# Performance work log

Measured on AMD Instinct MI355X. Metric: run time of the kernel, lower is better.

Reference implementation:

```python
import jax, jax.numpy as jnp
import numpy as np

D_MODEL = 1024
NUM_HEAD = 16
D_K = D_MODEL // NUM_HEAD


def setup_inputs() -> dict:
    key = jax.random.key(0)
    ks = jax.random.split(key, 9)
    s = 1.0 / np.sqrt(D_MODEL)
    return {
        "x": jax.random.normal(ks[0], (2, 2048, D_MODEL), dtype=jnp.float32),
        "Wq": jax.random.normal(ks[1], (D_MODEL, D_MODEL), dtype=jnp.float32) * s,
        "bq": jax.random.normal(ks[2], (D_MODEL,), dtype=jnp.float32) * s,
        "Wk": jax.random.normal(ks[3], (D_MODEL, D_MODEL), dtype=jnp.float32) * s,
        "bk": jax.random.normal(ks[4], (D_MODEL,), dtype=jnp.float32) * s,
        "Wv": jax.random.normal(ks[5], (D_MODEL, D_MODEL), dtype=jnp.float32) * s,
        "bv": jax.random.normal(ks[6], (D_MODEL,), dtype=jnp.float32) * s,
        "Wo": jax.random.normal(ks[7], (D_MODEL, D_MODEL), dtype=jnp.float32) * s,
        "bo": jax.random.normal(ks[8], (D_MODEL,), dtype=jnp.float32) * s,
    }


def reference(x, Wq, bq, Wk, bk, Wv, bv, Wo, bo):
    B, S, _ = x.shape
    # QKV projections: [B,S,D] -> [B,H,S,d_k]
    def proj(W, b):
        y = jnp.einsum("bsd,df->bsf", x, W) + b
        return y.reshape(B, S, NUM_HEAD, D_K).transpose(0, 2, 1, 3)

    Q = proj(Wq, bq)
    K = proj(Wk, bk)
    V = proj(Wv, bv)
    scale = 1.0 / jnp.sqrt(jnp.asarray(D_K, dtype=x.dtype))
    attn = jnp.einsum("bhqd,bhkd->bhqk", Q, K) * scale  # [B,H,S,S]
    probs = jax.nn.softmax(attn, axis=-1)
    out = jnp.einsum("bhqk,bhkd->bhqd", probs, V)  # [B,H,S,d_k]
    out = out.transpose(0, 2, 1, 3).reshape(B, S, D_MODEL)
    return jnp.einsum("bsd,df->bsf", out, Wo) + bo
```

## Files before the change

### kernel.cpp

```cpp
#include <hip/hip_runtime.h>
#include <hip/hip_bf16.h>
#include <math.h>

constexpr int DM = 1024;
constexpr int NH = 16;
constexpr int DK = 64;
constexpr int SQ = 2048;
constexpr int BB = 2;
constexpr int MR = BB * SQ;

typedef short bf16x8 __attribute__((ext_vector_type(8)));
typedef float f32x4 __attribute__((ext_vector_type(4)));
typedef float f32x16 __attribute__((ext_vector_type(16)));

__device__ inline unsigned short f2bf(float f) {
  unsigned u = __float_as_uint(f);
  unsigned r = (u + 0x7fffu + ((u >> 16) & 1u)) >> 16;
  return (unsigned short)r;
}

__device__ inline int fswz(int r) { return (r & 7) ^ ((r >> 3) & 7); }
__device__ inline int swz(int r, int c) {
  return r * 64 + ((((c >> 3) ^ fswz(r)) & 7) << 3) + (c & 7);
}
__device__ inline int vswz(int d, int c) {
  int g = c >> 3;
  g = (g & 24) | ((g ^ fswz(d)) & 7);
  return d * 256 + g * 8 + (c & 7);
}

__global__ __launch_bounds__(256)
void cast_kernel(const float* __restrict__ in, unsigned short* __restrict__ out, int n8) {
  int i = blockIdx.x * 256 + threadIdx.x;
  if (i >= n8) return;
  float4 a = *(const float4*)&in[(size_t)i * 8];
  float4 b = *(const float4*)&in[(size_t)i * 8 + 4];
  ushort4 lo = {f2bf(a.x), f2bf(a.y), f2bf(a.z), f2bf(a.w)};
  ushort4 hi = {f2bf(b.x), f2bf(b.y), f2bf(b.z), f2bf(b.w)};
  *(ushort4*)&out[(size_t)i * 8] = lo;
  *(ushort4*)&out[(size_t)i * 8 + 4] = hi;
}

__global__ __launch_bounds__(256)
void transpose_cast_kernel(const float* __restrict__ W, unsigned short* __restrict__ Wt) {
  __shared__ float tl[32][33];
  const int tx = threadIdx.x & 31, ty = threadIdx.x >> 5;
  const int x0 = blockIdx.x * 32, y0 = blockIdx.y * 32;
  #pragma unroll
  for (int i = 0; i < 4; ++i)
    tl[ty + i * 8][tx] = W[(size_t)(y0 + ty + i * 8) * DM + x0 + tx];
  __syncthreads();
  #pragma unroll
  for (int i = 0; i < 4; ++i)
    Wt[(size_t)(x0 + ty + i * 8) * DM + y0 + tx] = f2bf(tl[tx][ty + i * 8]);
}

__global__ __launch_bounds__(256)
void concat_bias(const float* __restrict__ bq, const float* __restrict__ bk,
                 const float* __restrict__ bv, float* __restrict__ cb) {
  int i = blockIdx.x * 256 + threadIdx.x;
  if (i < 1024) cb[i] = bq[i];
  else if (i < 2048) cb[i] = bk[i - 1024];
  else if (i < 3072) cb[i] = bv[i - 2048];
}

__global__ __launch_bounds__(256)
void transpose_v(const unsigned short* __restrict__ V, unsigned short* __restrict__ Vt) {
  __shared__ unsigned short tl[64 * 64];
  const int t = threadIdx.x;
  const int s0 = blockIdx.x * 64, bh = blockIdx.y;
  const unsigned short* src = V + (size_t)bh * SQ * DK;
  unsigned short* dst = Vt + (size_t)bh * DK * SQ;
  #pragma unroll
  for (int i = 0; i < 2; ++i) {
    int g = t + i * 256, r = g >> 3, cg = g & 7;
    uint4 v = *(const uint4*)&src[(size_t)(s0 + r) * DK + cg * 8];
    *(uint4*)&tl[r * 64 + (((cg ^ fswz(r)) & 7) << 3)] = v;
  }
  __syncthreads();
  #pragma unroll
  for (int i = 0; i < 2; ++i) {
    int g = t + i * 256, d = g >> 3, cs = g & 7;
    uint4 o;
    unsigned short* op = (unsigned short*)&o;
    #pragma unroll
    for (int e = 0; e < 8; ++e)
      op[e] = tl[swz(cs * 8 + e, d)];
    *(uint4*)&dst[(size_t)d * SQ + s0 + cs * 8] = o;
  }
}

__global__ __launch_bounds__(256)
void qkv_gemm(const unsigned short* __restrict__ A, const unsigned short* __restrict__ Wt3,
              const float* __restrict__ cbias, unsigned short* __restrict__ qkv)
{
  constexpr int K = DM;
  __shared__ unsigned short As[2][128 * 64];
  __shared__ unsigned short Bs[2][128 * 64];
  const int t = threadIdx.x;
  const int w = t >> 6, ln = t & 63;
  const int wr = w >> 1, wc = w & 1;
  const int rb = blockIdx.y * 128, cb = blockIdx.x * 128;

  f32x4 acc[4][4] = {};

  auto stage = [&](int buf, int k0) {
    #pragma unroll
    for (int j = 0; j < 4; ++j) {
      const int rows8 = (w * 4 + j) * 8;
      const int r = rows8 + (ln >> 3);
      const int gc = (((ln & 7) ^ fswz(r)) & 7) * 8;
      __builtin_amdgcn_global_load_lds(
          (const __attribute__((address_space(1))) void*)&A[(size_t)(rb + r) * K + k0 + gc],
          (__attribute__((address_space(3))) void*)&As[buf][rows8 * 64], 16, 0, 0);
      __builtin_amdgcn_global_load_lds(
          (const __attribute__((address_space(1))) void*)&Wt3[(size_t)(cb + r) * K + k0 + gc],
          (__attribute__((address_space(3))) void*)&Bs[buf][rows8 * 64], 16, 0, 0);
    }
  };

  stage(0, 0);
  asm volatile("s_waitcnt vmcnt(0)" ::: "memory");
  __builtin_amdgcn_s_barrier();

  for (int it = 0; it < K / 64; ++it) {
    const int buf = it & 1;
    if (it < K / 64 - 1) stage(buf ^ 1, (it + 1) * 64);
    const int rsel = ln & 15;
    #pragma unroll
    for (int kk = 0; kk < 2; ++kk) {
      const int ko = kk * 32 + (ln >> 4) * 8;
      bf16x8 af[4], bfr[4];
      #pragma unroll
      for (int m = 0; m < 4; ++m)
        af[m] = *(const bf16x8*)&As[buf][swz(wr * 64 + m * 16 + rsel, ko)];
      #pragma unroll
      for (int n = 0; n < 4; ++n)
        bfr[n] = *(const bf16x8*)&Bs[buf][swz(wc * 64 + n * 16 + rsel, ko)];
      #pragma unroll
      for (int m = 0; m < 4; ++m)
        #pragma unroll
        for (int n = 0; n < 4; ++n)
          acc[m][n] = __builtin_amdgcn_mfma_f32_16x16x32_bf16(af[m], bfr[n], acc[m][n], 0, 0, 0);
    }
    asm volatile("s_waitcnt vmcnt(0)" ::: "memory");
    __builtin_amdgcn_s_barrier();
  }

  const int cl = ln & 15, rg = (ln >> 4) * 4;
  const int which = cb >> 10;
  const float sc = (which == 0) ? 0.125f : 1.0f;
  unsigned short* dst0 = qkv + (size_t)which * MR * DM;
  #pragma unroll
  for (int m = 0; m < 4; ++m) {
    #pragma unroll
    for (int i = 0; i < 4; ++i) {
      const int r = rb + wr * 64 + m * 16 + rg + i;
      const int b = r >> 11, s = r & 2047;
      #pragma unroll
      for (int n = 0; n < 4; ++n) {
        const int c = cb + wc * 64 + n * 16 + cl;
        const float v = (acc[m][n][i] + cbias[c]) * sc;
        const int cc = c & 1023, h = cc >> 6, d = c & 63;
        dst0[(((size_t)(b * NH + h)) * SQ + s) * DK + d] = f2bf(v);
      }
    }
  }
}

__global__ __launch_bounds__(256)
void mfma_gemm_out(const unsigned short* __restrict__ A, const unsigned short* __restrict__ Bt,
                   const float* __restrict__ bias, float* __restrict__ outp)
{
  constexpr int K = DM, N = DM;
  __shared__ unsigned short As[2][128 * 64];
  __shared__ unsigned short Bs[2][128 * 64];
  const int t = threadIdx.x;
  const int w = t >> 6, ln = t & 63;
  const int wr = w >> 1, wc = w & 1;
  const int rb = blockIdx.y * 128, cb = blockIdx.x * 128;

  f32x4 acc[4][4] = {};

  auto stage = [&](int buf, int k0) {
    #pragma unroll
    for (int j = 0; j < 4; ++j) {
      const int rows8 = (w * 4 + j) * 8;
      const int r = rows8 + (ln >> 3);
      const int gc = (((ln & 7) ^ fswz(r)) & 7) * 8;
      __builtin_amdgcn_global_load_lds(
          (const __attribute__((address_space(1))) void*)&A[(size_t)(rb + r) * K + k0 + gc],
          (__attribute__((address_space(3))) void*)&As[buf][rows8 * 64], 16, 0, 0);
      __builtin_amdgcn_global_load_lds(
          (const __attribute__((address_space(1))) void*)&Bt[(size_t)(cb + r) * K + k0 + gc],
          (__attribute__((address_space(3))) void*)&Bs[buf][rows8 * 64], 16, 0, 0);
    }
  };

  stage(0, 0);
  asm volatile("s_waitcnt vmcnt(0)" ::: "memory");
  __builtin_amdgcn_s_barrier();

  for (int it = 0; it < K / 64; ++it) {
    const int buf = it & 1;
    if (it < K / 64 - 1) stage(buf ^ 1, (it + 1) * 64);
    const int rsel = ln & 15;
    #pragma unroll
    for (int kk = 0; kk < 2; ++kk) {
      const int ko = kk * 32 + (ln >> 4) * 8;
      bf16x8 af[4], bfr[4];
      #pragma unroll
      for (int m = 0; m < 4; ++m)
        af[m] = *(const bf16x8*)&As[buf][swz(wr * 64 + m * 16 + rsel, ko)];
      #pragma unroll
      for (int n = 0; n < 4; ++n)
        bfr[n] = *(const bf16x8*)&Bs[buf][swz(wc * 64 + n * 16 + rsel, ko)];
      #pragma unroll
      for (int m = 0; m < 4; ++m)
        #pragma unroll
        for (int n = 0; n < 4; ++n)
          acc[m][n] = __builtin_amdgcn_mfma_f32_16x16x32_bf16(af[m], bfr[n], acc[m][n], 0, 0, 0);
    }
    asm volatile("s_waitcnt vmcnt(0)" ::: "memory");
    __builtin_amdgcn_s_barrier();
  }

  const int cl = ln & 15, rg = (ln >> 4) * 4;
  #pragma unroll
  for (int m = 0; m < 4; ++m) {
    #pragma unroll
    for (int i = 0; i < 4; ++i) {
      const int r = rb + wr * 64 + m * 16 + rg + i;
      #pragma unroll
      for (int n = 0; n < 4; ++n) {
        const int c = cb + wc * 64 + n * 16 + cl;
        outp[(size_t)r * N + c] = acc[m][n][i] + bias[c];
      }
    }
  }
}

__global__ __launch_bounds__(512)
void attn_mfma32(const unsigned short* __restrict__ Qp, const unsigned short* __restrict__ Kp,
                 const unsigned short* __restrict__ VTp, unsigned short* __restrict__ ctx)
{
  __shared__ unsigned short Ks[256 * 64];
  __shared__ unsigned short Vt[64 * 256];
  const int t = threadIdx.x, w = t >> 6, ln = t & 63;
  const int lh = ln >> 5;
  const int bh = blockIdx.x, q0 = blockIdx.y * 256;
  const int b = bh >> 4, h = bh & 15;
  const unsigned short* Qb = Qp + (size_t)bh * SQ * DK;
  const unsigned short* Kb = Kp + (size_t)bh * SQ * DK;
  const unsigned short* Vb = VTp + (size_t)bh * DK * SQ;

  #pragma unroll
  for (int i = 0; i < 4; ++i) {
    int g = t + i * 512, r = g >> 3, cg = g & 7;
    uint4 qv = *(const uint4*)&Qb[(size_t)(q0 + r) * DK + cg * 8];
    *(uint4*)&Ks[r * 64 + (((cg ^ fswz(r)) & 7) << 3)] = qv;
  }
  __syncthreads();
  bf16x8 qf[4];
  #pragma unroll
  for (int s = 0; s < 4; ++s)
    qf[s] = *(const bf16x8*)&Ks[swz(w * 32 + (ln & 31), s * 16 + lh * 8)];
  __syncthreads();

  f32x16 o0 = {}, o1 = {};
  float m = -1e30f, l = 0.f;

  uint4 kr[4], vr[4];
  #pragma unroll
  for (int i = 0; i < 4; ++i) {
    int g = t + i * 512;
    kr[i] = *(const uint4*)&Kb[(size_t)(g >> 3) * DK + (g & 7) * 8];
    vr[i] = *(const uint4*)&Vb[(size_t)(g >> 5) * SQ + (g & 31) * 8];
  }
  #pragma unroll
  for (int i = 0; i < 4; ++i) {
    int g = t + i * 512, r = g >> 3, cg = g & 7;
    *(uint4*)&Ks[r * 64 + (((cg ^ fswz(r)) & 7) << 3)] = kr[i];
    int d = g >> 5, c = g & 31;
    *(uint4*)&Vt[d * 256 + (((c & 24) | ((c ^ fswz(d)) & 7)) << 3)] = vr[i];
  }
  __syncthreads();

  for (int oc = 0; oc < SQ / 256; ++oc) {
    const bool nxt = (oc + 1) < SQ / 256;
    if (nxt) {
      const int base = (oc + 1) * 256;
      #pragma unroll
      for (int i = 0; i < 4; ++i) {
        int g = t + i * 512;
        kr[i] = *(const uint4*)&Kb[(size_t)(base + (g >> 3)) * DK + (g & 7) * 8];
        vr[i] = *(const uint4*)&Vb[(size_t)(g >> 5) * SQ + base + (g & 31) * 8];
      }
    }

    #pragma unroll
    for (int it = 0; it < 4; ++it) {
      f32x16 s0 = {}, s1 = {};
      __builtin_amdgcn_s_setprio(1);
      #pragma unroll
      for (int s = 0; s < 4; ++s) {
        bf16x8 k0 = *(const bf16x8*)&Ks[swz(it * 64 + (ln & 31), s * 16 + lh * 8)];
        bf16x8 k1 = *(const bf16x8*)&Ks[swz(it * 64 + 32 + (ln & 31), s * 16 + lh * 8)];
        s0 = __builtin_amdgcn_mfma_f32_32x32x16_bf16(k0, qf[s], s0, 0, 0, 0);
        s1 = __builtin_amdgcn_mfma_f32_32x32x16_bf16(k1, qf[s], s1, 0, 0, 0);
      }
      __builtin_amdgcn_s_setprio(0);

      float mx0 = fmaxf(s0[0], s0[1]), mx1 = fmaxf(s0[2], s0[3]);
      #pragma unroll
      for (int j = 4; j < 16; j += 4) {
        mx0 = fmaxf(mx0, fmaxf(s0[j], s0[j + 1]));
        mx1 = fmaxf(mx1, fmaxf(s0[j + 2], s0[j + 3]));
      }
      #pragma unroll
      for (int j = 0; j < 16; j += 4) {
        mx0 = fmaxf(mx0, fmaxf(s1[j], s1[j + 1]));
        mx1 = fmaxf(mx1, fmaxf(s1[j + 2], s1[j + 3]));
      }
      float tm = fmaxf(mx0, mx1);
      tm = fmaxf(tm, __shfl_xor(tm, 32));

      if (__any((tm - m) > 8.f)) {
        const float mnew = fmaxf(m, tm);
        const float corr = __expf(m - mnew);
        float ci[16];
        #pragma unroll
        for (int j = 0; j < 16; ++j)
          ci[j] = __shfl(corr, (j & 3) + 8 * (j >> 2) + 4 * lh);
        #pragma unroll
        for (int j = 0; j < 16; ++j) { o0[j] *= ci[j]; o1[j] *= ci[j]; }
        l *= corr;
        m = mnew;
      }

      float p0[16], p1[16];
      #pragma unroll
      for (int j = 0; j < 16; ++j) {
        p0[j] = __expf(s0[j] - m);
        p1[j] = __expf(s1[j] - m);
      }
      float ps = 0.f;
      #pragma unroll
      for (int j = 0; j < 16; ++j) ps += p0[j] + p1[j];
      ps += __shfl_xor(ps, 32);
      l += ps;

      __builtin_amdgcn_s_setprio(1);
      #pragma unroll
      for (int s = 0; s < 4; ++s) {
        unsigned w0, w1, w2, w3;
        if (s == 0) {
          asm("v_cvt_pk_bf16_f32 %0, %1, %2" : "=v"(w0) : "v"(p0[0]), "v"(p0[1]));
          asm("v_cvt_pk_bf16_f32 %0, %1, %2" : "=v"(w1) : "v"(p0[2]), "v"(p0[3]));
          asm("v_cvt_pk_bf16_f32 %0, %1, %2" : "=v"(w2) : "v"(p0[4]), "v"(p0[5]));
          asm("v_cvt_pk_bf16_f32 %0, %1, %2" : "=v"(w3) : "v"(p0[6]), "v"(p0[7]));
        } else if (s == 1) {
          asm("v_cvt_pk_bf16_f32 %0, %1, %2" : "=v"(w0) : "v"(p0[8]), "v"(p0[9]));
          asm("v_cvt_pk_bf16_f32 %0, %1, %2" : "=v"(w1) : "v"(p0[10]), "v"(p0[11]));
          asm("v_cvt_pk_bf16_f32 %0, %1, %2" : "=v"(w2) : "v"(p0[12]), "v"(p0[13]));
          asm("v_cvt_pk_bf16_f32 %0, %1, %2" : "=v"(w3) : "v"(p0[14]), "v"(p0[15]));
        } else if (s == 2) {
          asm("v_cvt_pk_bf16_f32 %0, %1, %2" : "=v"(w0) : "v"(p1[0]), "v"(p1[1]));
          asm("v_cvt_pk_bf16_f32 %0, %1, %2" : "=v"(w1) : "v"(p1[2]), "v"(p1[3]));
          asm("v_cvt_pk_bf16_f32 %0, %1, %2" : "=v"(w2) : "v"(p1[4]), "v"(p1[5]));
          asm("v_cvt_pk_bf16_f32 %0, %1, %2" : "=v"(w3) : "v"(p1[6]), "v"(p1[7]));
        } else {
          asm("v_cvt_pk_bf16_f32 %0, %1, %2" : "=v"(w0) : "v"(p1[8]), "v"(p1[9]));
          asm("v_cvt_pk_bf16_f32 %0, %1, %2" : "=v"(w1) : "v"(p1[10]), "v"(p1[11]));
          asm("v_cvt_pk_bf16_f32 %0, %1, %2" : "=v"(w2) : "v"(p1[12]), "v"(p1[13]));
          asm("v_cvt_pk_bf16_f32 %0, %1, %2" : "=v"(w3) : "v"(p1[14]), "v"(p1[15]));
        }
        asm("v_permlane32_swap_b32 %0, %1" : "+v"(w0), "+v"(w2));
        asm("v_permlane32_swap_b32 %0, %1" : "+v"(w1), "+v"(w3));
        union { unsigned u[4]; bf16x8 v; } pa;
        pa.u[0] = w0; pa.u[1] = w1; pa.u[2] = w2; pa.u[3] = w3;
        bf16x8 v0 = *(const bf16x8*)&Vt[vswz(ln & 31, it * 64 + s * 16 + lh * 8)];
        bf16x8 v1 = *(const bf16x8*)&Vt[vswz(32 + (ln & 31), it * 64 + s * 16 + lh * 8)];
        o0 = __builtin_amdgcn_mfma_f32_32x32x16_bf16(pa.v, v0, o0, 0, 0, 0);
        o1 = __builtin_amdgcn_mfma_f32_32x32x16_bf16(pa.v, v1, o1, 0, 0, 0);
      }
      __builtin_amdgcn_s_setprio(0);
    }

    __syncthreads();
    if (nxt) {
      #pragma unroll
      for (int i = 0; i < 4; ++i) {
        int g = t + i * 512, r = g >> 3, cg = g & 7;
        *(uint4*)&Ks[r * 64 + (((cg ^ fswz(r)) & 7) << 3)] = kr[i];
        int d = g >> 5, c = g & 31;
        *(uint4*)&Vt[d * 256 + (((c & 24) | ((c ^ fswz(d)) & 7)) << 3)] = vr[i];
      }
      __syncthreads();
    }
  }

  const float rl = 1.0f / l;
  float ri[16];
  #pragma unroll
  for (int j = 0; j < 16; ++j)
    ri[j] = __shfl(rl, (j & 3) + 8 * (j >> 2) + 4 * lh);
  #pragma unroll
  for (int j = 0; j < 16; ++j) {
    const int srow = q0 + w * 32 + (j & 3) + 8 * (j >> 2) + 4 * lh;
    unsigned short* dst = ctx + ((size_t)(b * SQ + srow)) * DM + h * 64;
    dst[(ln & 31)]      = f2bf(o0[j] * ri[j]);
    dst[32 + (ln & 31)] = f2bf(o1[j] * ri[j]);
  }
}

extern "C" void kernel_launch(void* const* d_in, const int* in_sizes, int n_in,
                              void* d_out, int out_size, void* d_ws, size_t ws_size,
                              hipStream_t stream) {
  const float* x  = (const float*)d_in[0];
  const float* Wq = (const float*)d_in[1];
  const float* bq = (const float*)d_in[2];
  const float* Wk = (const float*)d_in[3];
  const float* bk = (const float*)d_in[4];
  const float* Wv = (const float*)d_in[5];
  const float* bv = (const float*)d_in[6];
  const float* Wo = (const float*)d_in[7];
  const float* bo = (const float*)d_in[8];
  float* out = (float*)d_out;

  unsigned short* xb    = (unsigned short*)d_ws;
  unsigned short* Wt3   = xb   + (size_t)MR * DM;
  unsigned short* Wto   = Wt3  + (size_t)3 * DM * DM;
  unsigned short* QKVb  = Wto  + (size_t)DM * DM;
  unsigned short* Vtb   = QKVb + (size_t)3 * MR * DM;
  unsigned short* ctxb  = Vtb  + (size_t)MR * DM;
  float*          cbias = (float*)(ctxb + (size_t)MR * DM);

  cast_kernel<<<(MR * DM / 8 + 255) / 256, 256, 0, stream>>>(x, xb, MR * DM / 8);
  dim3 tg(DM / 32, DM / 32);
  transpose_cast_kernel<<<tg, 256, 0, stream>>>(Wq, Wt3);
  transpose_cast_kernel<<<tg, 256, 0, stream>>>(Wk, Wt3 + (size_t)DM * DM);
  transpose_cast_kernel<<<tg, 256, 0, stream>>>(Wv, Wt3 + (size_t)2 * DM * DM);
  transpose_cast_kernel<<<tg, 256, 0, stream>>>(Wo, Wto);
  concat_bias<<<12, 256, 0, stream>>>(bq, bk, bv, cbias);

  qkv_gemm<<<dim3(3 * DM / 128, MR / 128), 256, 0, stream>>>(xb, Wt3, cbias, QKVb);
  transpose_v<<<dim3(SQ / 64, BB * NH), 256, 0, stream>>>(
      QKVb + (size_t)2 * MR * DM, Vtb);

  attn_mfma32<<<dim3(BB * NH, SQ / 256), 512, 0, stream>>>(
      QKVb, QKVb + (size_t)MR * DM, Vtb, ctxb);

  mfma_gemm_out<<<dim3(DM / 128, MR / 128), 256, 0, stream>>>(ctxb, Wto, bo, out);
}
```

Before: 170.0 us.

## Split attention KV range across two wave groups with async LDS double buffering

The attention kernel now launches 1024 threads per block, and two groups of 8 waves each process half of the key/value sequence for the same 256 query rows. K/V tiles are loaded directly into double-buffered LDS with global_load_lds, replacing register staging followed by an explicit store. At the end the two partial softmax states (m, l, O) are merged through LDS. The aim is more waves in flight to hide latency and less global-to-register-to-LDS copying. The cost is 128KB of LDS per block, which limits occupancy to one block per CU, plus the merge overhead.

```diff
diff --git a/kernel.cpp b/kernel.cpp
--- a/kernel.cpp
+++ b/kernel.cpp
@@ -23,11 +23,7 @@
 __device__ inline int swz(int r, int c) {
   return r * 64 + ((((c >> 3) ^ fswz(r)) & 7) << 3) + (c & 7);
 }
-__device__ inline int vswz(int d, int c) {
-  int g = c >> 3;
-  g = (g & 24) | ((g ^ fswz(d)) & 7);
-  return d * 256 + g * 8 + (c & 7);
-}
+__device__ inline int vslot(int d, int g) { return (g & 8) | ((g ^ fswz(d)) & 7); }
 
 __global__ __launch_bounds__(256)
 void cast_kernel(const float* __restrict__ in, unsigned short* __restrict__ out, int n8) {
@@ -240,72 +236,76 @@
   }
 }
 
-__global__ __launch_bounds__(512)
-void attn_mfma32(const unsigned short* __restrict__ Qp, const unsigned short* __restrict__ Kp,
-                 const unsigned short* __restrict__ VTp, unsigned short* __restrict__ ctx)
+__global__ __launch_bounds__(1024, 4)
+void attn_split(const unsigned short* __restrict__ Qp, const unsigned short* __restrict__ Kp,
+                const unsigned short* __restrict__ VTp, unsigned short* __restrict__ ctx)
 {
-  __shared__ unsigned short Ks[256 * 64];
-  __shared__ unsigned short Vt[64 * 256];
+  __shared__ unsigned short lds[65536];
   const int t = threadIdx.x, w = t >> 6, ln = t & 63;
   const int lh = ln >> 5;
+  const int part = w >> 3, qw = w & 7, tp = t & 511;
   const int bh = blockIdx.x, q0 = blockIdx.y * 256;
   const int b = bh >> 4, h = bh & 15;
   const unsigned short* Qb = Qp + (size_t)bh * SQ * DK;
   const unsigned short* Kb = Kp + (size_t)bh * SQ * DK;
   const unsigned short* Vb = VTp + (size_t)bh * DK * SQ;
-
-  #pragma unroll
-  for (int i = 0; i < 4; ++i) {
-    int g = t + i * 512, r = g >> 3, cg = g & 7;
+  const int kvbase = part * (SQ / 2);
+
+  #pragma unroll
+  for (int i = 0; i < 2; ++i) {
+    int g = t + i * 1024, r = g >> 3, cg = g & 7;
     uint4 qv = *(const uint4*)&Qb[(size_t)(q0 + r) * DK + cg * 8];
-    *(uint4*)&Ks[r * 64 + (((cg ^ fswz(r)) & 7) << 3)] = qv;
+    *(uint4*)&lds[r * 64 + (((cg ^ fswz(r)) & 7) << 3)] = qv;
   }
   __syncthreads();
   bf16x8 qf[4];
   #pragma unroll
   for (int s = 0; s < 4; ++s)
-    qf[s] = *(const bf16x8*)&Ks[swz(w * 32 + (ln & 31), s * 16 + lh * 8)];
+    qf[s] = *(const bf16x8*)&lds[swz(qw * 32 + (ln & 31), s * 16 + lh * 8)];
   __syncthreads();
+
+  unsigned short* KsB[2] = { lds + (part * 2 + 0) * 8192, lds + (part * 2 + 1) * 8192 };
+  unsigned short* VtB[2] = { lds + 32768 + (part * 2 + 0) * 8192,
+                             lds + 32768 + (part * 2 + 1) * 8192 };
 
   f32x16 o0 = {}, o1 = {};
   float m = -1e30f, l = 0.f;
 
-  uint4 kr[4], vr[4];
-  #pragma unroll
-  for (int i = 0; i < 4; ++i) {
-    int g = t + i * 512;
-    kr[i] = *(const uint4*)&Kb[(size_t)(g >> 3) * DK + (g & 7) * 8];
-    vr[i] = *(const uint4*)&Vb[(size_t)(g >> 5) * SQ + (g & 31) * 8];
-  }
-  #pragma unroll
-  for (int i = 0; i < 4; ++i) {
-    int g = t + i * 512, r = g >> 3, cg = g & 7;
-    *(uint4*)&Ks[r * 64 + (((cg ^ fswz(r)) & 7) << 3)] = kr[i];
-    int d = g >> 5, c = g & 31;
-    *(uint4*)&Vt[d * 256 + (((c & 24) | ((c ^ fswz(d)) & 7)) << 3)] = vr[i];
-  }
-  __syncthreads();
-
-  for (int oc = 0; oc < SQ / 256; ++oc) {
-    const bool nxt = (oc + 1) < SQ / 256;
-    if (nxt) {
-      const int base = (oc + 1) * 256;
-      #pragma unroll
-      for (int i = 0; i < 4; ++i) {
-        int g = t + i * 512;
-        kr[i] = *(const uint4*)&Kb[(size_t)(base + (g >> 3)) * DK + (g & 7) * 8];
-        vr[i] = *(const uint4*)&Vb[(size_t)(g >> 5) * SQ + base + (g & 31) * 8];
-      }
-    }
-
-    #pragma unroll
-    for (int it = 0; it < 4; ++it) {
+  auto stage = [&](int buf, int ck) {
+    #pragma unroll
+    for (int j = 0; j < 2; ++j) {
+      int g = tp + j * 512;
+      int r = g >> 3, gc = ((g & 7) ^ fswz(r)) & 7;
+      __builtin_amdgcn_global_load_lds(
+          (const __attribute__((address_space(1))) void*)
+              &Kb[(size_t)(kvbase + ck * 128 + r) * DK + gc * 8],
+          (__attribute__((address_space(3))) void*)(KsB[buf] + (qw * 64 + j * 512) * 8),
+          16, 0, 0);
+      int d = g >> 4, c = g & 15;
+      int cs = (c & 8) | ((c ^ fswz(d)) & 7);
+      __builtin_amdgcn_global_load_lds(
+          (const __attribute__((address_space(1))) void*)
+              &Vb[(size_t)d * SQ + kvbase + ck * 128 + cs * 8],
+          (__attribute__((address_space(3))) void*)(VtB[buf] + (qw * 64 + j * 512) * 8),
+          16, 0, 0);
+    }
+  };
+
+  stage(0, 0);
+  asm volatile("s_waitcnt vmcnt(0)" ::: "memory");
+  __builtin_amdgcn_s_barrier();
+
+  int buf = 0;
+  for (int ck = 0; ck < 8; ++ck) {
+    if (ck < 7) stage(buf ^ 1, ck + 1);
+    #pragma unroll
+    for (int it = 0; it < 2; ++it) {
       f32x16 s0 = {}, s1 = {};
       __builtin_amdgcn_s_setprio(1);
       #pragma unroll
       for (int s = 0; s < 4; ++s) {
-        bf16x8 k0 = *(const bf16x8*)&Ks[swz(it * 64 + (ln & 31), s * 16 + lh * 8)];
-        bf16x8 k1 = *(const bf16x8*)&Ks[swz(it * 64 + 32 + (ln & 31), s * 16 + lh * 8)];
+        bf16x8 k0 = *(const bf16x8*)&KsB[buf][swz(it * 64 + (ln & 31), s * 16 + lh * 8)];
+        bf16x8 k1 = *(const bf16x8*)&KsB[buf][swz(it * 64 + 32 + (ln & 31), s * 16 + lh * 8)];
         s0 = __builtin_amdgcn_mfma_f32_32x32x16_bf16(k0, qf[s], s0, 0, 0, 0);
         s1 = __builtin_amdgcn_mfma_f32_32x32x16_bf16(k1, qf[s], s1, 0, 0, 0);
       }
@@ -379,38 +379,50 @@
         asm("v_permlane32_swap_b32 %0, %1" : "+v"(w1), "+v"(w3));
         union { unsigned u[4]; bf16x8 v; } pa;
         pa.u[0] = w0; pa.u[1] = w1; pa.u[2] = w2; pa.u[3] = w3;
-        bf16x8 v0 = *(const bf16x8*)&Vt[vswz(ln & 31, it * 64 + s * 16 + lh * 8)];
-        bf16x8 v1 = *(const bf16x8*)&Vt[vswz(32 + (ln & 31), it * 64 + s * 16 + lh * 8)];
+        const int gx = it * 8 + s * 2 + lh;
+        bf16x8 v0 = *(const bf16x8*)&VtB[buf][(ln & 31) * 128 + vslot(ln & 31, gx) * 8];
+        bf16x8 v1 = *(const bf16x8*)&VtB[buf][(32 + (ln & 31)) * 128 + vslot(32 + (ln & 31), gx) * 8];
         o0 = __builtin_amdgcn_mfma_f32_32x32x16_bf16(pa.v, v0, o0, 0, 0, 0);
         o1 = __builtin_amdgcn_mfma_f32_32x32x16_bf16(pa.v, v1, o1, 0, 0, 0);
       }
       __builtin_amdgcn_s_setprio(0);
     }
-
-    __syncthreads();
-    if (nxt) {
-      #pragma unroll
-      for (int i = 0; i < 4; ++i) {
-        int g = t + i * 512, r = g >> 3, cg = g & 7;
-        *(uint4*)&Ks[r * 64 + (((cg ^ fswz(r)) & 7) << 3)] = kr[i];
-        int d = g >> 5, c = g & 31;
-        *(uint4*)&Vt[d * 256 + (((c & 24) | ((c ^ fswz(d)) & 7)) << 3)] = vr[i];
-      }
-      __syncthreads();
-    }
-  }
-
-  const float rl = 1.0f / l;
-  float ri[16];
-  #pragma unroll
-  for (int j = 0; j < 16; ++j)
-    ri[j] = __shfl(rl, (j & 3) + 8 * (j >> 2) + 4 * lh);
-  #pragma unroll
-  for (int j = 0; j < 16; ++j) {
-    const int srow = q0 + w * 32 + (j & 3) + 8 * (j >> 2) + 4 * lh;
-    unsigned short* dst = ctx + ((size_t)(b * SQ + srow)) * DM + h * 64;
-    dst[(ln & 31)]      = f2bf(o0[j] * ri[j]);
-    dst[32 + (ln & 31)] = f2bf(o1[j] * ri[j]);
+    asm volatile("s_waitcnt vmcnt(0)" ::: "memory");
+    __builtin_amdgcn_s_barrier();
+    buf ^= 1;
+  }
+
+  float* Obuf = (float*)lds;
+  float* mlb  = (float*)&lds[32768];
+  if (part == 1) {
+    #pragma unroll
+    for (int j = 0; j < 16; ++j) {
+      Obuf[qw * 2048 + j * 64 + ln]        = o0[j];
+      Obuf[qw * 2048 + (16 + j) * 64 + ln] = o1[j];
+    }
+    mlb[qw * 128 + ln * 2]     = m;
+    mlb[qw * 128 + ln * 2 + 1] = l;
+  }
+  __syncthreads();
+  if (part == 0) {
+    const float m1 = mlb[qw * 128 + ln * 2];
+    const float l1 = mlb[qw * 128 + ln * 2 + 1];
+    const float M  = fmaxf(m, m1);
+    const float e0 = __expf(m - M), e1 = __expf(m1 - M);
+    const float rl = 1.0f / (l * e0 + l1 * e1);
+    const float f0 = e0 * rl, f1 = e1 * rl;
+    #pragma unroll
+    for (int j = 0; j < 16; ++j) {
+      const int crow = (j & 3) + 8 * (j >> 2) + 4 * lh;
+      const float a0 = __shfl(f0, crow);
+      const float a1 = __shfl(f1, crow);
+      const float v0 = o0[j] * a0 + Obuf[qw * 2048 + j * 64 + ln] * a1;
+      const float v1 = o1[j] * a0 + Obuf[qw * 2048 + (16 + j) * 64 + ln] * a1;
+      const int srow = q0 + qw * 32 + crow;
+      unsigned short* dst = ctx + ((size_t)(b * SQ + srow)) * DM + h * 64;
+      dst[ln & 31]        = f2bf(v0);
+      dst[32 + (ln & 31)] = f2bf(v1);
+    }
   }
 }
 
@@ -448,7 +460,7 @@
   transpose_v<<<dim3(SQ / 64, BB * NH), 256, 0, stream>>>(
       QKVb + (size_t)2 * MR * DM, Vtb);
 
-  attn_mfma32<<<dim3(BB * NH, SQ / 256), 512, 0, stream>>>(
+  attn_split<<<dim3(BB * NH, SQ / 256), 1024, 0, stream>>>(
       QKVb, QKVb + (size_t)MR * DM, Vtb, ctxb);
 
   mfma_gemm_out<<<dim3(DM / 128, MR / 128), 256, 0, stream>>>(ctxb, Wto, bo, out);
```

Result: slower. 317.8 us (+86.9%).
